# Performance work log

Hardware: AMD Instinct MI355X
Metric: run time of the kernel (lower is better)

Reference implementation:

```python
import jax, jax.numpy as jnp
import numpy as np

W_BIT = 4
HALF = 2 ** (W_BIT - 1)  # 8: recentering offset used in post_init
GROUP_SIZE = 128
IN_FEATURES = 4096
OUT_FEATURES = 11008
TOKENS = 32


def setup_inputs() -> dict:
    key = jax.random.key(0)
    k1, k2, k3, k4, k5 = jax.random.split(key, 5)
    n_groups = IN_FEATURES // GROUP_SIZE
    x = jax.random.normal(k1, (TOKENS, IN_FEATURES), dtype=jnp.float32)
    # unpacked 4-bit weight codes in [0, 15]
    qweight = jax.random.randint(k2, (IN_FEATURES, OUT_FEATURES), 0, 2 ** W_BIT, dtype=jnp.int32)
    # group-wise 4-bit zero-point codes in [0, 15]
    qzeros = jax.random.randint(k3, (n_groups, OUT_FEATURES), 0, 2 ** W_BIT, dtype=jnp.int32)
    # group-wise scales (positive, small, like real quant scales)
    scales = jax.random.uniform(k4, (n_groups, OUT_FEATURES), dtype=jnp.float32, minval=0.001, maxval=0.02)
    bias = jax.random.normal(k5, (OUT_FEATURES,), dtype=jnp.float32)
    return {"x": x, "qweight": qweight, "qzeros": qzeros, "scales": scales, "bias": bias}


def reference(x, qweight, qzeros, scales, bias):
    # post_init recenters codes: q -> q - 2^(b-1), z -> z - 2^(b-1)
    w_int = (qweight - HALF).astype(jnp.float32)            # [K, N]
    z_int = (qzeros - HALF).astype(jnp.float32)             # [K//gs, N]
    # broadcast group-wise zeros/scales along K
    z_rep = jnp.repeat(z_int, GROUP_SIZE, axis=0)           # [K, N]
    s_rep = jnp.repeat(scales, GROUP_SIZE, axis=0)          # [K, N]
    # fused dequant-GEMM: y = x @ ((q - z) * s) + bias
    w_deq = (w_int - z_rep) * s_rep                         # [K, N] fp32
    out = x @ w_deq + bias                                  # [T, N]
    return out
```

## Files before the change

kernel.cpp:

```cpp
#include <hip/hip_runtime.h>
#include <hip/hip_bf16.h>


#define TOKENS   32
#define KDIM     4096
#define NDIM     11008
#define GS       128
#define KSPLIT   32
#define KCHUNK   128
#define BLOCK    128
#define COLS     2
#define NB       (NDIM / (BLOCK * COLS))

__global__ __launch_bounds__(256) void awq_xpose_kernel(
    const float* __restrict__ x, float* __restrict__ xT)
{
    __shared__ float tile[64 * 33];
    const int tid = threadIdx.x;
    const int k0  = blockIdx.x * 64;
    const int kk  = tid & 63;
    const int tq  = tid >> 6;
    #pragma unroll
    for (int i = 0; i < 8; ++i) {
        const int t = tq + 4 * i;
        tile[kk * 33 + t] = x[t * KDIM + k0 + kk];
    }
    __syncthreads();
    #pragma unroll
    for (int i = 0; i < 8; ++i) {
        const int o  = tid + 256 * i;
        const int t  = o & 31;
        const int k  = o >> 5;
        xT[(k0 + k) * TOKENS + t] = tile[k * 33 + t];
    }
}

__global__ __launch_bounds__(256) void awq_init_kernel(
    const float* __restrict__ bias, float* __restrict__ out)
{
    const int n = blockIdx.x * 256 + threadIdx.x;
    out[blockIdx.y * NDIM + n] = bias[n];
}

template<bool ATOMIC>
__global__ __launch_bounds__(BLOCK) void awq_gemm_kernel(
    const float* __restrict__ xT,
    const int*   __restrict__ qw,
    const int*   __restrict__ qz,
    const float* __restrict__ sc,
    float*       __restrict__ dst)
{
    const int tid = threadIdx.x;
    const int kc0 = blockIdx.y * KCHUNK;
    const int n0  = blockIdx.x * (BLOCK * COLS) + tid * COLS;

    const int grp = blockIdx.y;
    const float2 s2 = *(const float2*)&sc[(size_t)grp * NDIM + n0];
    const int2   z2 = *(const int2*)  &qz[(size_t)grp * NDIM + n0];
    const float nzs0 = -(float)z2.x * s2.x;
    const float nzs1 = -(float)z2.y * s2.y;

    float acc0[TOKENS], acc1[TOKENS];
    #pragma unroll
    for (int t = 0; t < TOKENS; ++t) { acc0[t] = 0.f; acc1[t] = 0.f; }

    const int2* qp = (const int2*)(qw + (size_t)kc0 * NDIM + n0);

    #pragma unroll 2
    for (int k = 0; k < KCHUNK; ++k) {
        const int2 q = qp[(size_t)k * (NDIM / 2)];
        const float w0 = fmaf((float)q.x, s2.x, nzs0);
        const float w1 = fmaf((float)q.y, s2.y, nzs1);

        const float4* xk = (const float4*)(xT + (size_t)(kc0 + k) * TOKENS);
        #pragma unroll
        for (int j = 0; j < 8; ++j) {
            const float4 xv = xk[j];
            acc0[j*4+0] = fmaf(w0, xv.x, acc0[j*4+0]);
            acc1[j*4+0] = fmaf(w1, xv.x, acc1[j*4+0]);
            acc0[j*4+1] = fmaf(w0, xv.y, acc0[j*4+1]);
            acc1[j*4+1] = fmaf(w1, xv.y, acc1[j*4+1]);
            acc0[j*4+2] = fmaf(w0, xv.z, acc0[j*4+2]);
            acc1[j*4+2] = fmaf(w1, xv.z, acc1[j*4+2]);
            acc0[j*4+3] = fmaf(w0, xv.w, acc0[j*4+3]);
            acc1[j*4+3] = fmaf(w1, xv.w, acc1[j*4+3]);
        }
    }

    if (ATOMIC) {
        float* op = dst + n0;
        #pragma unroll
        for (int t = 0; t < TOKENS; ++t) {
            unsafeAtomicAdd(op + (size_t)t * NDIM + 0, acc0[t]);
            unsafeAtomicAdd(op + (size_t)t * NDIM + 1, acc1[t]);
        }
    } else {
        float* pp = dst + ((size_t)blockIdx.y * TOKENS) * NDIM + n0;
        #pragma unroll
        for (int t = 0; t < TOKENS; ++t) {
            *(float2*)(pp + (size_t)t * NDIM) = make_float2(acc0[t], acc1[t]);
        }
    }
}

__global__ __launch_bounds__(256) void awq_reduce_kernel(
    const float* __restrict__ part,
    const float* __restrict__ bias,
    float*       __restrict__ out)
{
    const int o = blockIdx.x * 256 + threadIdx.x;
    const int t = o / (NDIM / 4);
    const int c = o - t * (NDIM / 4);
    const float4* p4 = (const float4*)part;
    float4 sum = ((const float4*)bias)[c];
    #pragma unroll
    for (int s = 0; s < KSPLIT; ++s) {
        const float4 v = p4[(size_t)(s * TOKENS + t) * (NDIM / 4) + c];
        sum.x += v.x; sum.y += v.y; sum.z += v.z; sum.w += v.w;
    }
    ((float4*)out)[o] = sum;
}

extern "C" void kernel_launch(void* const* d_in, const int* in_sizes, int n_in,
                              void* d_out, int out_size, void* d_ws, size_t ws_size,
                              hipStream_t stream) {
    const float* x    = (const float*)d_in[0];
    const int*   qw   = (const int*)  d_in[1];
    const int*   qz   = (const int*)  d_in[2];
    const float* sc   = (const float*)d_in[3];
    const float* bias = (const float*)d_in[4];
    float* out = (float*)d_out;

    const size_t xt_bytes   = (size_t)KDIM * TOKENS * sizeof(float);
    const size_t part_bytes = (size_t)KSPLIT * TOKENS * NDIM * sizeof(float);
    float* xT   = (float*)d_ws;
    float* part = (float*)((char*)d_ws + xt_bytes);

    awq_xpose_kernel<<<KDIM / 64, 256, 0, stream>>>(x, xT);

    if (ws_size >= xt_bytes + part_bytes) {
        awq_gemm_kernel<false><<<dim3(NB, KSPLIT), BLOCK, 0, stream>>>(
            xT, qw, qz, sc, part);
        awq_reduce_kernel<<<(TOKENS * NDIM / 4) / 256, 256, 0, stream>>>(
            part, bias, out);
    } else {
        awq_init_kernel<<<dim3(NDIM / 256, TOKENS), 256, 0, stream>>>(bias, out);
        awq_gemm_kernel<true><<<dim3(NB, KSPLIT), BLOCK, 0, stream>>>(
            xT, qw, qz, sc, out);
    }
}
```

Baseline: 291.7 us.

## Replace scalar FP32 dequant-GEMM with bf16 MFMA 16x16x32 tiles

Activations are converted to bf16 in a small pre-kernel instead of being transposed. The main kernel now has each wave dequantize a 64-column by 32-K slab of weights into bf16 registers and feed `mfma_f32_16x16x32_bf16` instructions, covering all 32 tokens in two M tiles. This aims to move the multiply-accumulate work off scalar FP32 FMAs onto the matrix cores, which were the likely bottleneck. In exchange, both activations and dequantized weights are rounded to bf16, which adds numerical error. The reduce loop's unroll is also reduced.

Measured after the change: 279.2 us. 4.3% less time.

```diff
diff --git a/kernel.cpp b/kernel.cpp
--- a/kernel.cpp
+++ b/kernel.cpp
@@ -8,31 +8,30 @@
 #define GS       128
 #define KSPLIT   32
 #define KCHUNK   128
-#define BLOCK    128
-#define COLS     2
-#define NB       (NDIM / (BLOCK * COLS))
+#define BLOCK    256
+#define WAVE_N   64
+#define BLOCK_N  256
 
-__global__ __launch_bounds__(256) void awq_xpose_kernel(
-    const float* __restrict__ x, float* __restrict__ xT)
+typedef __attribute__((ext_vector_type(8))) short short8;
+typedef __attribute__((ext_vector_type(4))) float floatx4;
+
+__device__ __forceinline__ short f2bf(float f) {
+    unsigned u = __builtin_bit_cast(unsigned, f);
+    u += 0x7fffu + ((u >> 16) & 1u);
+    return (short)(u >> 16);
+}
+
+__global__ __launch_bounds__(256) void awq_cvt_kernel(
+    const float* __restrict__ x, unsigned short* __restrict__ xb)
 {
-    __shared__ float tile[64 * 33];
-    const int tid = threadIdx.x;
-    const int k0  = blockIdx.x * 64;
-    const int kk  = tid & 63;
-    const int tq  = tid >> 6;
-    #pragma unroll
-    for (int i = 0; i < 8; ++i) {
-        const int t = tq + 4 * i;
-        tile[kk * 33 + t] = x[t * KDIM + k0 + kk];
-    }
-    __syncthreads();
-    #pragma unroll
-    for (int i = 0; i < 8; ++i) {
-        const int o  = tid + 256 * i;
-        const int t  = o & 31;
-        const int k  = o >> 5;
-        xT[(k0 + k) * TOKENS + t] = tile[k * 33 + t];
-    }
+    const int i = blockIdx.x * 256 + threadIdx.x;
+    const float4 v = ((const float4*)x)[i];
+    ushort4 o;
+    o.x = (unsigned short)f2bf(v.x);
+    o.y = (unsigned short)f2bf(v.y);
+    o.z = (unsigned short)f2bf(v.z);
+    o.w = (unsigned short)f2bf(v.w);
+    ((ushort4*)xb)[i] = o;
 }
 
 __global__ __launch_bounds__(256) void awq_init_kernel(
@@ -43,63 +42,86 @@
 }
 
 template<bool ATOMIC>
-__global__ __launch_bounds__(BLOCK) void awq_gemm_kernel(
-    const float* __restrict__ xT,
+__global__ __launch_bounds__(BLOCK) void awq_gemm_mfma(
+    const unsigned short* __restrict__ xb,
     const int*   __restrict__ qw,
     const int*   __restrict__ qz,
     const float* __restrict__ sc,
     float*       __restrict__ dst)
 {
-    const int tid = threadIdx.x;
-    const int kc0 = blockIdx.y * KCHUNK;
-    const int n0  = blockIdx.x * (BLOCK * COLS) + tid * COLS;
+    const int tid  = threadIdx.x;
+    const int lane = tid & 63;
+    const int wv   = tid >> 6;
+    const int col  = lane & 15;
+    const int quad = lane >> 4;
+    const int g    = blockIdx.y;
+    const int kc0  = g * KCHUNK;
+    const int nb   = blockIdx.x * BLOCK_N + wv * WAVE_N;
 
-    const int grp = blockIdx.y;
-    const float2 s2 = *(const float2*)&sc[(size_t)grp * NDIM + n0];
-    const int2   z2 = *(const int2*)  &qz[(size_t)grp * NDIM + n0];
-    const float nzs0 = -(float)z2.x * s2.x;
-    const float nzs1 = -(float)z2.y * s2.y;
+    float s[4], nzs[4];
+    #pragma unroll
+    for (int nt = 0; nt < 4; ++nt) {
+        const int n  = nb + nt * 16 + col;
+        const float sv = sc[(size_t)g * NDIM + n];
+        const int   zv = qz[(size_t)g * NDIM + n];
+        s[nt] = sv; nzs[nt] = -(float)zv * sv;
+    }
 
-    float acc0[TOKENS], acc1[TOKENS];
+    floatx4 acc[4][2];
     #pragma unroll
-    for (int t = 0; t < TOKENS; ++t) { acc0[t] = 0.f; acc1[t] = 0.f; }
+    for (int nt = 0; nt < 4; ++nt) {
+        acc[nt][0] = (floatx4){0.f, 0.f, 0.f, 0.f};
+        acc[nt][1] = (floatx4){0.f, 0.f, 0.f, 0.f};
+    }
 
-    const int2* qp = (const int2*)(qw + (size_t)kc0 * NDIM + n0);
+    const int* qp = qw + (size_t)(kc0 + quad * 8) * NDIM + nb + col;
+    const unsigned short* xr0 = xb + (size_t)col * KDIM + kc0 + quad * 8;
+    const unsigned short* xr1 = xr0 + 16 * KDIM;
 
     #pragma unroll 2
-    for (int k = 0; k < KCHUNK; ++k) {
-        const int2 q = qp[(size_t)k * (NDIM / 2)];
-        const float w0 = fmaf((float)q.x, s2.x, nzs0);
-        const float w1 = fmaf((float)q.y, s2.y, nzs1);
+    for (int ks = 0; ks < KCHUNK / 32; ++ks) {
+        int q[4][8];
+        #pragma unroll
+        for (int nt = 0; nt < 4; ++nt)
+            #pragma unroll
+            for (int j = 0; j < 8; ++j)
+                q[nt][j] = qp[(ks * 32 + j) * NDIM + nt * 16];
 
-        const float4* xk = (const float4*)(xT + (size_t)(kc0 + k) * TOKENS);
+        const short8 a0 = *(const short8*)(xr0 + ks * 32);
+        const short8 a1 = *(const short8*)(xr1 + ks * 32);
+
         #pragma unroll
-        for (int j = 0; j < 8; ++j) {
-            const float4 xv = xk[j];
-            acc0[j*4+0] = fmaf(w0, xv.x, acc0[j*4+0]);
-            acc1[j*4+0] = fmaf(w1, xv.x, acc1[j*4+0]);
-            acc0[j*4+1] = fmaf(w0, xv.y, acc0[j*4+1]);
-            acc1[j*4+1] = fmaf(w1, xv.y, acc1[j*4+1]);
-            acc0[j*4+2] = fmaf(w0, xv.z, acc0[j*4+2]);
-            acc1[j*4+2] = fmaf(w1, xv.z, acc1[j*4+2]);
-            acc0[j*4+3] = fmaf(w0, xv.w, acc0[j*4+3]);
-            acc1[j*4+3] = fmaf(w1, xv.w, acc1[j*4+3]);
+        for (int nt = 0; nt < 4; ++nt) {
+            short8 b;
+            #pragma unroll
+            for (int j = 0; j < 8; ++j)
+                b[j] = f2bf(fmaf((float)q[nt][j], s[nt], nzs[nt]));
+            acc[nt][0] = __builtin_amdgcn_mfma_f32_16x16x32_bf16(a0, b, acc[nt][0], 0, 0, 0);
+            acc[nt][1] = __builtin_amdgcn_mfma_f32_16x16x32_bf16(a1, b, acc[nt][1], 0, 0, 0);
         }
     }
 
     if (ATOMIC) {
-        float* op = dst + n0;
         #pragma unroll
-        for (int t = 0; t < TOKENS; ++t) {
-            unsafeAtomicAdd(op + (size_t)t * NDIM + 0, acc0[t]);
-            unsafeAtomicAdd(op + (size_t)t * NDIM + 1, acc1[t]);
-        }
+        for (int nt = 0; nt < 4; ++nt)
+            #pragma unroll
+            for (int h = 0; h < 2; ++h) {
+                float* pp = dst + (size_t)(h * 16 + quad * 4) * NDIM + nb + nt * 16 + col;
+                #pragma unroll
+                for (int r = 0; r < 4; ++r)
+                    unsafeAtomicAdd(pp + (size_t)r * NDIM, acc[nt][h][r]);
+            }
     } else {
-        float* pp = dst + ((size_t)blockIdx.y * TOKENS) * NDIM + n0;
+        float* pbase = dst + (size_t)g * TOKENS * NDIM;
         #pragma unroll
-        for (int t = 0; t < TOKENS; ++t) {
-            *(float2*)(pp + (size_t)t * NDIM) = make_float2(acc0[t], acc1[t]);
-        }
+        for (int nt = 0; nt < 4; ++nt)
+            #pragma unroll
+            for (int h = 0; h < 2; ++h) {
+                float* pp = pbase + (size_t)(h * 16 + quad * 4) * NDIM + nb + nt * 16 + col;
+                #pragma unroll
+                for (int r = 0; r < 4; ++r)
+                    pp[(size_t)r * NDIM] = acc[nt][h][r];
+            }
     }
 }
 
@@ -113,7 +135,7 @@
     const int c = o - t * (NDIM / 4);
     const float4* p4 = (const float4*)part;
     float4 sum = ((const float4*)bias)[c];
-    #pragma unroll
+    #pragma unroll 8
     for (int s = 0; s < KSPLIT; ++s) {
         const float4 v = p4[(size_t)(s * TOKENS + t) * (NDIM / 4) + c];
         sum.x += v.x; sum.y += v.y; sum.z += v.z; sum.w += v.w;
@@ -131,21 +153,21 @@
     const float* bias = (const float*)d_in[4];
     float* out = (float*)d_out;
 
-    const size_t xt_bytes   = (size_t)KDIM * TOKENS * sizeof(float);
+    const size_t xb_bytes   = 512 * 1024;
     const size_t part_bytes = (size_t)KSPLIT * TOKENS * NDIM * sizeof(float);
-    float* xT   = (float*)d_ws;
-    float* part = (float*)((char*)d_ws + xt_bytes);
+    unsigned short* xb = (unsigned short*)d_ws;
+    float* part = (float*)((char*)d_ws + xb_bytes);
 
-    awq_xpose_kernel<<<KDIM / 64, 256, 0, stream>>>(x, xT);
+    awq_cvt_kernel<<<(TOKENS * KDIM / 4) / 256, 256, 0, stream>>>(x, xb);
 
-    if (ws_size >= xt_bytes + part_bytes) {
-        awq_gemm_kernel<false><<<dim3(NB, KSPLIT), BLOCK, 0, stream>>>(
-            xT, qw, qz, sc, part);
+    if (ws_size >= xb_bytes + part_bytes) {
+        awq_gemm_mfma<false><<<dim3(NDIM / BLOCK_N, KSPLIT), BLOCK, 0, stream>>>(
+            xb, qw, qz, sc, part);
         awq_reduce_kernel<<<(TOKENS * NDIM / 4) / 256, 256, 0, stream>>>(
             part, bias, out);
     } else {
         awq_init_kernel<<<dim3(NDIM / 256, TOKENS), 256, 0, stream>>>(bias, out);
-        awq_gemm_kernel<true><<<dim3(NB, KSPLIT), BLOCK, 0, stream>>>(
-            xT, qw, qz, sc, out);
+        awq_gemm_mfma<true><<<dim3(NDIM / BLOCK_N, KSPLIT), BLOCK, 0, stream>>>(
+            xb, qw, qz, sc, out);
     }
 }
```
